# Performance work log

Measured on AMD Instinct MI355X. Metric: run time of the kernel, lower is better.

Reference implementation:

```python
import jax, jax.numpy as jnp
import numpy as np

NUM_NODES = 17185
D = 6
FEATS = NUM_NODES * D  # 103110
BATCH = 256
EPS = 1e-5


def setup_inputs() -> dict:
    key = jax.random.key(0)
    ks = jax.random.split(key, 4)
    data = jax.random.normal(ks[0], (BATCH, FEATS), dtype=jnp.float32)
    w_blocks = jax.random.normal(ks[1], (NUM_NODES, D, D), dtype=jnp.float32) * (1.0 / np.sqrt(D))
    b_blocks = jax.random.normal(ks[2], (NUM_NODES, D), dtype=jnp.float32) * 0.1
    fc_w = jax.random.normal(ks[3], (FEATS,), dtype=jnp.float32) * (1.0 / np.sqrt(FEATS))
    return {
        "data": data,
        "w_blocks": w_blocks,
        "b_blocks": b_blocks,
        "bn_gamma": jnp.ones((FEATS,), jnp.float32),
        "bn_beta": jnp.zeros((FEATS,), jnp.float32),
        "bn_mean": jnp.zeros((FEATS,), jnp.float32),
        "bn_var": jnp.ones((FEATS,), jnp.float32),
        "fc_w": fc_w,
        "fc_b": jnp.zeros((1,), jnp.float32),
        "bnf_gamma": jnp.ones((1,), jnp.float32),
        "bnf_beta": jnp.zeros((1,), jnp.float32),
        "bnf_mean": jnp.zeros((1,), jnp.float32),
        "bnf_var": jnp.ones((1,), jnp.float32),
    }


def reference(data, w_blocks, b_blocks, bn_gamma, bn_beta, bn_mean, bn_var,
              fc_w, fc_b, bnf_gamma, bnf_beta, bnf_mean, bnf_var):
    B = data.shape[0]
    # block-diagonal batched matmul replacing 17185 tiny Linear(6,6) calls
    x = data.reshape(B, NUM_NODES, D)                       # [B, N, 6]
    xo = jnp.einsum("bni,noi->bno", x, w_blocks) + b_blocks  # torch Linear: x @ W^T + b
    xo = xo.reshape(B, FEATS)                               # hstack ordering == reshape
    # relu -> BatchNorm1d (eval: running stats) -> dropout (identity in eval)
    h = jnp.maximum(xo, 0.0)
    h = (h - bn_mean) * jax.lax.rsqrt(bn_var + EPS) * bn_gamma + bn_beta
    # final linear [FEATS -> 1], BN(1), sigmoid
    y = h @ fc_w + fc_b                                     # [B]
    y = y[:, None]                                          # [B, 1]
    y = (y - bnf_mean) * jax.lax.rsqrt(bnf_var + EPS) * bnf_gamma + bnf_beta
    return jax.nn.sigmoid(y)
```

## Files before the change

kernel.cpp:

```cpp
#include <hip/hip_runtime.h>
#include <stdint.h>

#define NUM_NODES 17185
#define DD 6
#define FEATS (NUM_NODES * DD)
#define BATCH 256
#define EPS 1e-5f

#define NC 256
#define BC 8
#define NCHUNK ((NUM_NODES + NC - 1) / NC)
#define CPREP_BLOCKS 256


__global__ __launch_bounds__(256) void cprep_kernel(
    const float* __restrict__ beta, const float* __restrict__ mean,
    const float* __restrict__ gamma, const float* __restrict__ var,
    const float* __restrict__ fcw, float* __restrict__ pc) {
    int tid = blockIdx.x * blockDim.x + threadIdx.x;
    int stride = gridDim.x * blockDim.x;
    float local = 0.f;
    for (int f = tid; f < FEATS; f += stride) {
        float sc = gamma[f] * rsqrtf(var[f] + EPS);
        local += (beta[f] - mean[f] * sc) * fcw[f];
    }
    #pragma unroll
    for (int off = 32; off; off >>= 1) local += __shfl_down(local, off);
    __shared__ float red[4];
    if ((threadIdx.x & 63) == 0) red[threadIdx.x >> 6] = local;
    __syncthreads();
    if (threadIdx.x == 0) pc[blockIdx.x] = red[0] + red[1] + red[2] + red[3];
}

__global__ __launch_bounds__(NC) void main_kernel(
    const float* __restrict__ data, const float* __restrict__ wb, const float* __restrict__ bb,
    const float* __restrict__ gamma, const float* __restrict__ var, const float* __restrict__ fcw,
    float* __restrict__ pm) {

    const int tid = threadIdx.x;
    const int n = blockIdx.x * NC + tid;
    const bool valid = (n < NUM_NODES);

    float wreg[36], bias[6], a[6];
    #pragma unroll
    for (int k = 0; k < 36; k++) wreg[k] = 0.f;
    #pragma unroll
    for (int k = 0; k < 6; k++) { bias[k] = 0.f; a[k] = 0.f; }

    if (valid) {
        const float4* wp = (const float4*)(wb + (size_t)n * 36);
        #pragma unroll
        for (int k = 0; k < 9; k++) {
            float4 v = wp[k];
            wreg[4*k] = v.x; wreg[4*k+1] = v.y; wreg[4*k+2] = v.z; wreg[4*k+3] = v.w;
        }
        const float2* bp = (const float2*)(bb + (size_t)n * 6);
        #pragma unroll
        for (int k = 0; k < 3; k++) { float2 v = bp[k]; bias[2*k] = v.x; bias[2*k+1] = v.y; }
        const int f0 = n * 6;
        const float2* gp = (const float2*)(gamma + f0);
        const float2* vp = (const float2*)(var + f0);
        const float2* fp = (const float2*)(fcw + f0);
        #pragma unroll
        for (int k = 0; k < 3; k++) {
            float2 g = gp[k], v = vp[k], f = fp[k];
            a[2*k]   = g.x * rsqrtf(v.x + EPS) * f.x;
            a[2*k+1] = g.y * rsqrtf(v.y + EPS) * f.y;
        }
    }

    const int b0 = blockIdx.y * BC;
    float acc[BC];
    #pragma unroll
    for (int r = 0; r < BC; r++) acc[r] = 0.f;

    if (valid) {
        const float2* xbase = (const float2*)(data + (size_t)b0 * FEATS + (size_t)n * 6);
        #pragma unroll
        for (int r = 0; r < BC; r++) {
            const float2* xp = xbase + (size_t)r * (FEATS / 2);
            float2 u0 = xp[0], u1 = xp[1], u2 = xp[2];
            float x0 = u0.x, x1 = u0.y, x2 = u1.x, x3 = u1.y, x4 = u2.x, x5 = u2.y;
            float s;
            #pragma unroll
            for (int o = 0; o < 6; o++) {
                s = bias[o];
                s = fmaf(x0, wreg[o*6+0], s);
                s = fmaf(x1, wreg[o*6+1], s);
                s = fmaf(x2, wreg[o*6+2], s);
                s = fmaf(x3, wreg[o*6+3], s);
                s = fmaf(x4, wreg[o*6+4], s);
                s = fmaf(x5, wreg[o*6+5], s);
                acc[r] = fmaf(fmaxf(s, 0.f), a[o], acc[r]);
            }
        }
    }

    __shared__ float red[4][BC];
    #pragma unroll
    for (int r = 0; r < BC; r++) {
        float v = acc[r];
        #pragma unroll
        for (int off = 32; off; off >>= 1) v += __shfl_down(v, off);
        if ((tid & 63) == 0) red[tid >> 6][r] = v;
    }
    __syncthreads();
    if (tid < BC) {
        float s = red[0][tid] + red[1][tid] + red[2][tid] + red[3][tid];
        pm[blockIdx.x * 256 + b0 + tid] = s;
    }
}

__global__ __launch_bounds__(256) void final_kernel(
    const float* __restrict__ pm, const float* __restrict__ pc,
    const float* __restrict__ fcb, const float* __restrict__ bnfg,
    const float* __restrict__ bnfb, const float* __restrict__ bnfm,
    const float* __restrict__ bnfv, float* __restrict__ out) {
    const int b = threadIdx.x;

    float c = pc[b];
    #pragma unroll
    for (int off = 32; off; off >>= 1) c += __shfl_down(c, off);
    __shared__ float red[4];
    if ((b & 63) == 0) red[b >> 6] = c;
    __syncthreads();
    const float c_sum = red[0] + red[1] + red[2] + red[3];

    float y = 0.f;
    for (int ch = 0; ch < NCHUNK; ch++) y += pm[ch * 256 + b];

    y += c_sum + fcb[0];
    float sc = bnfg[0] * rsqrtf(bnfv[0] + EPS);
    float z = (y - bnfm[0]) * sc + bnfb[0];
    out[b] = 1.f / (1.f + expf(-z));
}

extern "C" void kernel_launch(void* const* d_in, const int* in_sizes, int n_in,
                              void* d_out, int out_size, void* d_ws, size_t ws_size,
                              hipStream_t stream) {
    const float* data  = (const float*)d_in[0];
    const float* wb    = (const float*)d_in[1];
    const float* bb    = (const float*)d_in[2];
    const float* gamma = (const float*)d_in[3];
    const float* beta  = (const float*)d_in[4];
    const float* mean  = (const float*)d_in[5];
    const float* var   = (const float*)d_in[6];
    const float* fcw   = (const float*)d_in[7];
    const float* fcb   = (const float*)d_in[8];
    const float* bnfg  = (const float*)d_in[9];
    const float* bnfb  = (const float*)d_in[10];
    const float* bnfm  = (const float*)d_in[11];
    const float* bnfv  = (const float*)d_in[12];

    float* pm = (float*)d_ws;
    float* pc = pm + NCHUNK * 256;

    cprep_kernel<<<CPREP_BLOCKS, 256, 0, stream>>>(beta, mean, gamma, var, fcw, pc);

    dim3 grid(NCHUNK, BATCH / BC);
    main_kernel<<<grid, NC, 0, stream>>>(data, wb, bb, gamma, var, fcw, pm);

    final_kernel<<<1, 256, 0, stream>>>(pm, pc, fcb, bnfg, bnfb, bnfm, bnfv, (float*)d_out);
}
```

Measured before the change: 191.6 us.

## Fuse constant-term prep kernel into main kernel and double batch chunk

Removes the separate cprep kernel and computes the per-node constant term (beta - mean*scale)*fc_w inside the main kernel's y==0 blocks, reducing it per block into pc. The batch chunk per block grows from 8 to 16, halving the grid's y dimension and amortizing weight/parameter loads over more rows. This saves one kernel launch and redundant parameter reads, at the cost of more registers per thread and fewer blocks for latency hiding.

```diff
diff --git a/kernel.cpp b/kernel.cpp
--- a/kernel.cpp
+++ b/kernel.cpp
@@ -8,34 +8,15 @@
 #define EPS 1e-5f
 
 #define NC 256
-#define BC 8
+#define BC 16
 #define NCHUNK ((NUM_NODES + NC - 1) / NC)
-#define CPREP_BLOCKS 256
 
-
-__global__ __launch_bounds__(256) void cprep_kernel(
-    const float* __restrict__ beta, const float* __restrict__ mean,
-    const float* __restrict__ gamma, const float* __restrict__ var,
-    const float* __restrict__ fcw, float* __restrict__ pc) {
-    int tid = blockIdx.x * blockDim.x + threadIdx.x;
-    int stride = gridDim.x * blockDim.x;
-    float local = 0.f;
-    for (int f = tid; f < FEATS; f += stride) {
-        float sc = gamma[f] * rsqrtf(var[f] + EPS);
-        local += (beta[f] - mean[f] * sc) * fcw[f];
-    }
-    #pragma unroll
-    for (int off = 32; off; off >>= 1) local += __shfl_down(local, off);
-    __shared__ float red[4];
-    if ((threadIdx.x & 63) == 0) red[threadIdx.x >> 6] = local;
-    __syncthreads();
-    if (threadIdx.x == 0) pc[blockIdx.x] = red[0] + red[1] + red[2] + red[3];
-}
 
 __global__ __launch_bounds__(NC) void main_kernel(
     const float* __restrict__ data, const float* __restrict__ wb, const float* __restrict__ bb,
     const float* __restrict__ gamma, const float* __restrict__ var, const float* __restrict__ fcw,
-    float* __restrict__ pm) {
+    const float* __restrict__ beta, const float* __restrict__ mean,
+    float* __restrict__ pm, float* __restrict__ pc) {
 
     const int tid = threadIdx.x;
     const int n = blockIdx.x * NC + tid;
@@ -46,6 +27,8 @@
     for (int k = 0; k < 36; k++) wreg[k] = 0.f;
     #pragma unroll
     for (int k = 0; k < 6; k++) { bias[k] = 0.f; a[k] = 0.f; }
+
+    float cnode = 0.f;
 
     if (valid) {
         const float4* wp = (const float4*)(wb + (size_t)n * 36);
@@ -61,11 +44,23 @@
         const float2* gp = (const float2*)(gamma + f0);
         const float2* vp = (const float2*)(var + f0);
         const float2* fp = (const float2*)(fcw + f0);
+        float fw[6];
         #pragma unroll
         for (int k = 0; k < 3; k++) {
             float2 g = gp[k], v = vp[k], f = fp[k];
+            fw[2*k] = f.x; fw[2*k+1] = f.y;
             a[2*k]   = g.x * rsqrtf(v.x + EPS) * f.x;
             a[2*k+1] = g.y * rsqrtf(v.y + EPS) * f.y;
+        }
+        if (blockIdx.y == 0) {
+            const float2* bep = (const float2*)(beta + f0);
+            const float2* mp  = (const float2*)(mean + f0);
+            #pragma unroll
+            for (int k = 0; k < 3; k++) {
+                float2 be = bep[k], m = mp[k];
+                cnode += be.x * fw[2*k]   - m.x * a[2*k];
+                cnode += be.y * fw[2*k+1] - m.y * a[2*k+1];
+            }
         }
     }
 
@@ -81,10 +76,9 @@
             const float2* xp = xbase + (size_t)r * (FEATS / 2);
             float2 u0 = xp[0], u1 = xp[1], u2 = xp[2];
             float x0 = u0.x, x1 = u0.y, x2 = u1.x, x3 = u1.y, x4 = u2.x, x5 = u2.y;
-            float s;
             #pragma unroll
             for (int o = 0; o < 6; o++) {
-                s = bias[o];
+                float s = bias[o];
                 s = fmaf(x0, wreg[o*6+0], s);
                 s = fmaf(x1, wreg[o*6+1], s);
                 s = fmaf(x2, wreg[o*6+2], s);
@@ -104,7 +98,19 @@
         for (int off = 32; off; off >>= 1) v += __shfl_down(v, off);
         if ((tid & 63) == 0) red[tid >> 6][r] = v;
     }
-    __syncthreads();
+
+    if (blockIdx.y == 0) {
+        float v = cnode;
+        #pragma unroll
+        for (int off = 32; off; off >>= 1) v += __shfl_down(v, off);
+        __shared__ float credd[4];
+        if ((tid & 63) == 0) credd[tid >> 6] = v;
+        __syncthreads();
+        if (tid == 0) pc[blockIdx.x] = credd[0] + credd[1] + credd[2] + credd[3];
+    } else {
+        __syncthreads();
+    }
+
     if (tid < BC) {
         float s = red[0][tid] + red[1][tid] + red[2][tid] + red[3][tid];
         pm[blockIdx.x * 256 + b0 + tid] = s;
@@ -118,7 +124,7 @@
     const float* __restrict__ bnfv, float* __restrict__ out) {
     const int b = threadIdx.x;
 
-    float c = pc[b];
+    float c = (b < NCHUNK) ? pc[b] : 0.f;
     #pragma unroll
     for (int off = 32; off; off >>= 1) c += __shfl_down(c, off);
     __shared__ float red[4];
@@ -127,6 +133,7 @@
     const float c_sum = red[0] + red[1] + red[2] + red[3];
 
     float y = 0.f;
+    #pragma unroll 4
     for (int ch = 0; ch < NCHUNK; ch++) y += pm[ch * 256 + b];
 
     y += c_sum + fcb[0];
@@ -155,10 +162,8 @@
     float* pm = (float*)d_ws;
     float* pc = pm + NCHUNK * 256;
 
-    cprep_kernel<<<CPREP_BLOCKS, 256, 0, stream>>>(beta, mean, gamma, var, fcw, pc);
-
     dim3 grid(NCHUNK, BATCH / BC);
-    main_kernel<<<grid, NC, 0, stream>>>(data, wb, bb, gamma, var, fcw, pm);
+    main_kernel<<<grid, NC, 0, stream>>>(data, wb, bb, gamma, var, fcw, beta, mean, pm, pc);
 
     final_kernel<<<1, 256, 0, stream>>>(pm, pc, fcb, bnfg, bnfb, bnfm, bnfv, (float*)d_out);
 }
```

Measured after the change: 191.4 us. No clear change (-0.1%).
